# Performance work log

Hardware: AMD Instinct MI355X
Metric: run time of the kernel (lower is better)

The kernel has to match this reference:

```python
import jax, jax.numpy as jnp
import numpy as np

TANH_CLIP = 10.0
TEMP = 1.0


def setup_inputs() -> dict:
    key = jax.random.key(0)
    ks = jax.random.split(key, 8)
    B, N, E, H, SC = 1024, 1000, 128, 8, 256
    dk = E // H
    context = jax.random.normal(ks[0], (B, 1, E), dtype=jnp.float32)
    step_context = jax.random.normal(ks[1], (B, 1, SC), dtype=jnp.float32)
    # scale weights so tanh/softmax stay in a sane numeric range
    W_step = jax.random.normal(ks[2], (E, SC), dtype=jnp.float32) * 0.05
    glimpse_K = jax.random.normal(ks[3], (H, B, 1, N, dk), dtype=jnp.float32)
    glimpse_V = jax.random.normal(ks[4], (H, B, 1, N, dk), dtype=jnp.float32)
    logit_K = jax.random.normal(ks[5], (B, 1, N, E), dtype=jnp.float32)
    W_out = jax.random.normal(ks[6], (E, E), dtype=jnp.float32) * 0.05
    mask = jax.random.randint(ks[7], (B, 1, N), 0, 2).astype(bool)
    mask = mask.at[:, :, 0].set(False)  # guarantee at least one feasible node
    return {"context": context, "step_context": step_context, "W_step": W_step,
            "glimpse_K": glimpse_K, "glimpse_V": glimpse_V, "logit_K": logit_K,
            "W_out": W_out, "mask": mask}


def reference(context, step_context, W_step, glimpse_K, glimpse_V, logit_K, W_out, mask):
    B, S, E = context.shape          # S = num_steps = 1
    H = glimpse_K.shape[0]
    dk = E // H
    neg_inf = jnp.float32(-jnp.inf)
    # query = context_node_projected + project_step_context(step_context)
    query = context + jnp.einsum('bsc,ec->bse', step_context, W_step)  # [B,S,E]
    # split heads: glimpse_Q -> [H,B,S,dk] (the singleton q-dim of the torch code is folded)
    Q = query.reshape(B, S, H, dk).transpose(2, 0, 1, 3)
    # compatibility [H,B,S,N]
    compat = jnp.einsum('hbsk,hbsnk->hbsn', Q, glimpse_K) / jnp.sqrt(jnp.float32(dk))
    compat = jnp.where(mask[None], neg_inf, compat)       # mask_inner
    attn = jax.nn.softmax(compat, axis=-1)
    heads = jnp.einsum('hbsn,hbsnk->hbsk', attn, glimpse_V)  # [H,B,S,dk]
    glimpse = heads.transpose(1, 2, 0, 3).reshape(B, S, E)   # concat heads
    glimpse = jnp.einsum('bse,oe->bso', glimpse, W_out)      # project_out
    # logits against logit_K  [B,S,N]
    logits = jnp.einsum('bse,bsne->bsn', glimpse, logit_K) / jnp.sqrt(jnp.float32(E))
    logits = jnp.tanh(logits) * jnp.float32(TANH_CLIP)       # tanh clipping
    logits = jnp.where(mask, neg_inf, logits)                # mask_logits
    log_p = jax.nn.log_softmax(logits / jnp.float32(TEMP), axis=-1)
    return log_p
```

## Files before the change

### kernel.cpp

```cpp
#include <hip/hip_runtime.h>
#include <hip/hip_bf16.h>
#include <math.h>

#define NB  1024
#define NN  1000
#define NE  128
#define NH  8
#define NDK 16
#define NSC 256

__global__ __launch_bounds__(128)
void query_kernel(const float* __restrict__ ctx, const float* __restrict__ stepc,
                  const float* __restrict__ Wstep, float* __restrict__ q_ws)
{
    const int b = blockIdx.x, t = threadIdx.x;
    __shared__ float sc[NSC];
    sc[t] = stepc[b * NSC + t];
    sc[t + 128] = stepc[b * NSC + t + 128];
    __syncthreads();
    float acc = ctx[b * NE + t];
    const float4* w4 = reinterpret_cast<const float4*>(Wstep + t * NSC);
    #pragma unroll 8
    for (int c4 = 0; c4 < NSC / 4; ++c4) {
        float4 w = w4[c4];
        acc += sc[4*c4] * w.x + sc[4*c4+1] * w.y + sc[4*c4+2] * w.z + sc[4*c4+3] * w.w;
    }
    q_ws[b * NE + t] = acc;
}

__global__ __launch_bounds__(256)
void attn_kernel(const float* __restrict__ q_ws, const float* __restrict__ gK,
                 const float* __restrict__ gV, const unsigned char* __restrict__ mask,
                 float* __restrict__ heads_ws)
{
    const int bid = blockIdx.x;
    const int h = bid >> 10;
    const int b = bid & (NB - 1);
    const int t = threadIdx.x;
    const int w = t >> 6, lane = t & 63;

    __shared__ float wmax[4], wsum[4], wred[64];
    __shared__ int mtype;

    if (t == 0) {
        const unsigned int* mi = reinterpret_cast<const unsigned int*>(mask);
        int ok = 1;
        for (int i = 0; i < 64; ++i) ok = ok && (mi[i] <= 1u);
        mtype = ok;
    }
    __syncthreads();
    const int m_i32 = mtype;
    const int* mask_i = reinterpret_cast<const int*>(mask);

    const float4* q4 = reinterpret_cast<const float4*>(q_ws + b * NE + h * NDK);
    float4 q0 = q4[0], q1 = q4[1], q2 = q4[2], q3 = q4[3];

    const float* Kbase = gK + ((size_t)h * NB + b) * NN * NDK;
    const float* Vbase = gV + ((size_t)h * NB + b) * NN * NDK;

    float sc[4];
    #pragma unroll
    for (int i = 0; i < 4; ++i) {
        const int n = t + i * 256;
        float v = -INFINITY;
        if (n < NN) {
            bool mk = m_i32 ? (mask_i[b * NN + n] != 0) : (mask[b * NN + n] != 0);
            if (!mk) {
                const float4* k4 = reinterpret_cast<const float4*>(Kbase + (size_t)n * NDK);
                float4 k0 = k4[0], k1 = k4[1], k2 = k4[2], k3 = k4[3];
                float acc = k0.x*q0.x + k0.y*q0.y + k0.z*q0.z + k0.w*q0.w
                          + k1.x*q1.x + k1.y*q1.y + k1.z*q1.z + k1.w*q1.w
                          + k2.x*q2.x + k2.y*q2.y + k2.z*q2.z + k2.w*q2.w
                          + k3.x*q3.x + k3.y*q3.y + k3.z*q3.z + k3.w*q3.w;
                v = acc * 0.25f;
            }
        }
        sc[i] = v;
    }

    float m = fmaxf(fmaxf(sc[0], sc[1]), fmaxf(sc[2], sc[3]));
    #pragma unroll
    for (int off = 32; off > 0; off >>= 1) m = fmaxf(m, __shfl_down(m, off));
    if (lane == 0) wmax[w] = m;
    __syncthreads();
    const float M = fmaxf(fmaxf(wmax[0], wmax[1]), fmaxf(wmax[2], wmax[3]));

    float e[4], s = 0.f;
    #pragma unroll
    for (int i = 0; i < 4; ++i) { e[i] = expf(sc[i] - M); s += e[i]; }
    #pragma unroll
    for (int off = 32; off > 0; off >>= 1) s += __shfl_down(s, off);
    if (lane == 0) wsum[w] = s;
    __syncthreads();
    const float rinv = 1.0f / (wsum[0] + wsum[1] + wsum[2] + wsum[3]);

    float acc[16];
    #pragma unroll
    for (int k = 0; k < 16; ++k) acc[k] = 0.f;
    #pragma unroll
    for (int i = 0; i < 4; ++i) {
        const int n = t + i * 256;
        const float p = e[i];
        if (n < NN && p != 0.f) {
            const float4* v4 = reinterpret_cast<const float4*>(Vbase + (size_t)n * NDK);
            float4 v0 = v4[0], v1 = v4[1], v2 = v4[2], v3 = v4[3];
            acc[0]+=p*v0.x; acc[1]+=p*v0.y; acc[2]+=p*v0.z; acc[3]+=p*v0.w;
            acc[4]+=p*v1.x; acc[5]+=p*v1.y; acc[6]+=p*v1.z; acc[7]+=p*v1.w;
            acc[8]+=p*v2.x; acc[9]+=p*v2.y; acc[10]+=p*v2.z; acc[11]+=p*v2.w;
            acc[12]+=p*v3.x; acc[13]+=p*v3.y; acc[14]+=p*v3.z; acc[15]+=p*v3.w;
        }
    }
    #pragma unroll
    for (int k = 0; k < 16; ++k) {
        float a = acc[k];
        #pragma unroll
        for (int off = 32; off > 0; off >>= 1) a += __shfl_down(a, off);
        acc[k] = a;
    }
    if (lane < 16) wred[w * 16 + lane] = acc[lane];
    __syncthreads();
    if (lane == 0) {
        #pragma unroll
        for (int k = 0; k < 16; ++k) wred[w * 16 + k] = acc[k];
    }
    __syncthreads();
    if (t < NDK) {
        float r = wred[t] + wred[16 + t] + wred[32 + t] + wred[48 + t];
        heads_ws[b * NE + h * NDK + t] = r * rinv;
    }
}

__global__ __launch_bounds__(256)
void logits_kernel(const float* __restrict__ heads_ws, const float* __restrict__ Wout,
                   const float* __restrict__ lK, const unsigned char* __restrict__ mask,
                   __hip_bfloat16* __restrict__ out)
{
    const int b = blockIdx.x, t = threadIdx.x;
    __shared__ __align__(16) float g[NE];
    __shared__ __align__(16) float gout[NE];
    __shared__ __align__(16) float llds[NN];
    __shared__ __align__(16) float red[256];
    __shared__ float Mv, Sv;
    __shared__ int mtype;

    if (t == 0) {
        const unsigned int* mi = reinterpret_cast<const unsigned int*>(mask);
        int ok = 1;
        for (int i = 0; i < 64; ++i) ok = ok && (mi[i] <= 1u);
        mtype = ok;
    }
    if (t < NE) g[t] = heads_ws[b * NE + t];
    __syncthreads();
    const int m_i32 = mtype;
    const int* mask_i = reinterpret_cast<const int*>(mask);

    if (t < NE) {
        float acc = 0.f;
        const float4* w4 = reinterpret_cast<const float4*>(Wout + t * NE);
        const float4* g4 = reinterpret_cast<const float4*>(g);
        #pragma unroll 8
        for (int e4 = 0; e4 < NE / 4; ++e4) {
            float4 wv = w4[e4]; float4 gg = g4[e4];
            acc += wv.x*gg.x + wv.y*gg.y + wv.z*gg.z + wv.w*gg.w;
        }
        gout[t] = acc;
    }
    __syncthreads();

    for (int n = t; n < NN; n += 256) {
        bool mk = m_i32 ? (mask_i[b * NN + n] != 0) : (mask[b * NN + n] != 0);
        float val;
        if (mk) {
            val = -3.0e38f;
        } else {
            const float4* lk4 = reinterpret_cast<const float4*>(lK + ((size_t)b * NN + n) * NE);
            const float4* go4 = reinterpret_cast<const float4*>(gout);
            float acc = 0.f;
            #pragma unroll 8
            for (int e4 = 0; e4 < NE / 4; ++e4) {
                float4 lv = lk4[e4]; float4 gv = go4[e4];
                acc += lv.x*gv.x + lv.y*gv.y + lv.z*gv.z + lv.w*gv.w;
            }
            val = tanhf(acc * 0.08838834764831845f) * 10.0f;
        }
        llds[n] = val;
    }
    __syncthreads();

    float m = -INFINITY;
    for (int n = t; n < NN; n += 256) m = fmaxf(m, llds[n]);
    red[t] = m;
    __syncthreads();
    for (int s2 = 128; s2 > 0; s2 >>= 1) {
        if (t < s2) red[t] = fmaxf(red[t], red[t + s2]);
        __syncthreads();
    }
    if (t == 0) Mv = red[0];
    __syncthreads();
    const float M = Mv;
    float s = 0.f;
    for (int n = t; n < NN; n += 256) s += expf(llds[n] - M);
    red[t] = s;
    __syncthreads();
    for (int s2 = 128; s2 > 0; s2 >>= 1) {
        if (t < s2) red[t] += red[t + s2];
        __syncthreads();
    }
    if (t == 0) Sv = logf(red[0]);
    __syncthreads();
    const float LS = M + Sv;
    for (int n = t; n < NN; n += 256) {
        out[(size_t)b * NN + n] = __float2bfloat16(llds[n] - LS);
    }
}

__global__ __launch_bounds__(256, 4)
void evrp_decoder_fused(const float* __restrict__ ctx, const float* __restrict__ stepc,
                        const float* __restrict__ Wstep, const float* __restrict__ gK,
                        const float* __restrict__ gV, const float* __restrict__ lK,
                        const float* __restrict__ Wout, const unsigned char* __restrict__ mask,
                        __hip_bfloat16* __restrict__ out)
{
    const int b = blockIdx.x;
    const int t = threadIdx.x;
    __shared__ __align__(16) float q[NE];
    __shared__ __align__(16) float sc_l[NH * NN];
    __shared__ __align__(16) float g[NE];
    __shared__ __align__(16) float gout[NE];
    __shared__ __align__(16) float red[256];
    __shared__ __align__(16) float ovl[1024];
    __shared__ float mh[NH];
    __shared__ float rinv[NH];
    __shared__ float Mv, Sv;
    __shared__ int mtype;

    if (t == 0) {
        const unsigned int* mi = reinterpret_cast<const unsigned int*>(mask);
        int ok = 1;
        for (int i = 0; i < 64; ++i) ok = ok && (mi[i] <= 1u);
        mtype = ok;
    }
    red[t] = stepc[b * NSC + t];
    __syncthreads();
    const int m_i32 = mtype;
    if (t < NE) {
        float acc = ctx[b * NE + t];
        const float4* w4 = reinterpret_cast<const float4*>(Wstep + t * NSC);
        #pragma unroll 8
        for (int c4 = 0; c4 < NSC / 4; ++c4) {
            float4 w = w4[c4];
            acc += red[c4*4+0]*w.x + red[c4*4+1]*w.y + red[c4*4+2]*w.z + red[c4*4+3]*w.w;
        }
        q[t] = acc;
    }
    __syncthreads();
    const int* mask_i = reinterpret_cast<const int*>(mask);
    for (int n = t; n < NN; n += 256) {
        bool mk = m_i32 ? (mask_i[b * NN + n] != 0) : (mask[b * NN + n] != 0);
        if (mk) {
            #pragma unroll
            for (int h = 0; h < NH; ++h) sc_l[h * NN + n] = -INFINITY;
        } else {
            #pragma unroll
            for (int h = 0; h < NH; ++h) {
                const float4* k4 = reinterpret_cast<const float4*>(gK + (((size_t)h*NB + b)*NN + n)*NDK);
                const float4* q4 = reinterpret_cast<const float4*>(q + h * NDK);
                float acc = 0.f;
                #pragma unroll
                for (int i = 0; i < 4; ++i) {
                    float4 kv = k4[i]; float4 qv = q4[i];
                    acc += kv.x*qv.x + kv.y*qv.y + kv.z*qv.z + kv.w*qv.w;
                }
                sc_l[h * NN + n] = acc * 0.25f;
            }
        }
    }
    __syncthreads();
    {
        const int h = t >> 5, i = t & 31;
        float m = -INFINITY;
        for (int n = i; n < NN; n += 32) m = fmaxf(m, sc_l[h * NN + n]);
        red[t] = m;
        __syncthreads();
        if (t < NH) {
            float mm = -INFINITY;
            for (int i2 = 0; i2 < 32; ++i2) mm = fmaxf(mm, red[t * 32 + i2]);
            mh[t] = mm;
        }
        __syncthreads();
        const float mhh = mh[h];
        float s = 0.f;
        for (int n = i; n < NN; n += 32) {
            float ev = expf(sc_l[h * NN + n] - mhh);
            sc_l[h * NN + n] = ev;
            s += ev;
        }
        red[t] = s;
        __syncthreads();
        if (t < NH) {
            float ss = 0.f;
            for (int i2 = 0; i2 < 32; ++i2) ss += red[t * 32 + i2];
            rinv[t] = 1.0f / ss;
        }
        __syncthreads();
    }
    {
        float4* hp4 = reinterpret_cast<float4*>(ovl);
        const int h = t >> 5, rem = t & 31, kq = rem >> 3, j = rem & 7;
        const float* vbase = gV + (((size_t)h * NB + b) * NN) * NDK + kq * 4;
        float4 acc = {0.f, 0.f, 0.f, 0.f};
        for (int n = j; n < NN; n += 8) {
            float p = sc_l[h * NN + n];
            if (p != 0.f) {
                float4 v = *reinterpret_cast<const float4*>(vbase + (size_t)n * NDK);
                acc.x += p*v.x; acc.y += p*v.y; acc.z += p*v.z; acc.w += p*v.w;
            }
        }
        hp4[(h * 4 + kq) * 8 + j] = acc;
    }
    __syncthreads();
    if (t < NE) {
        const int h = t >> 4, k = t & 15, kq = k >> 2, kc = k & 3;
        float s = 0.f;
        #pragma unroll
        for (int j = 0; j < 8; ++j) s += ovl[((h * 4 + kq) * 8 + j) * 4 + kc];
        g[t] = s * rinv[h];
    }
    __syncthreads();
    if (t < NE) {
        float acc = 0.f;
        const float4* w4 = reinterpret_cast<const float4*>(Wout + t * NE);
        const float4* g4 = reinterpret_cast<const float4*>(g);
        #pragma unroll 8
        for (int e4 = 0; e4 < NE / 4; ++e4) {
            float4 w = w4[e4]; float4 gg = g4[e4];
            acc += w.x*gg.x + w.y*gg.y + w.z*gg.z + w.w*gg.w;
        }
        gout[t] = acc;
    }
    __syncthreads();
    float* llds = ovl;
    for (int n = t; n < NN; n += 256) {
        bool mk = m_i32 ? (mask_i[b * NN + n] != 0) : (mask[b * NN + n] != 0);
        float val;
        if (mk) val = -INFINITY;
        else {
            const float4* lk4 = reinterpret_cast<const float4*>(lK + ((size_t)b * NN + n) * NE);
            const float4* go4 = reinterpret_cast<const float4*>(gout);
            float acc = 0.f;
            #pragma unroll 8
            for (int e4 = 0; e4 < NE / 4; ++e4) {
                float4 lv = lk4[e4]; float4 gv = go4[e4];
                acc += lv.x*gv.x + lv.y*gv.y + lv.z*gv.z + lv.w*gv.w;
            }
            val = tanhf(acc * 0.08838834764831845f) * 10.0f;
        }
        llds[n] = val;
    }
    __syncthreads();
    {
        float m = -INFINITY;
        for (int n = t; n < NN; n += 256) m = fmaxf(m, llds[n]);
        red[t] = m;
        __syncthreads();
        for (int s2 = 128; s2 > 0; s2 >>= 1) {
            if (t < s2) red[t] = fmaxf(red[t], red[t + s2]);
            __syncthreads();
        }
        if (t == 0) Mv = red[0];
        __syncthreads();
        const float M = Mv;
        float s = 0.f;
        for (int n = t; n < NN; n += 256) s += expf(llds[n] - M);
        red[t] = s;
        __syncthreads();
        for (int s2 = 128; s2 > 0; s2 >>= 1) {
            if (t < s2) red[t] += red[t + s2];
            __syncthreads();
        }
        if (t == 0) Sv = logf(red[0]);
        __syncthreads();
        const float LS = M + Sv;
        for (int n = t; n < NN; n += 256) {
            float l = llds[n];
            float r = (l == -INFINITY) ? -3.0e38f : (l - LS);
            out[(size_t)b * NN + n] = __float2bfloat16(r);
        }
    }
}

extern "C" void kernel_launch(void* const* d_in, const int* in_sizes, int n_in,
                              void* d_out, int out_size, void* d_ws, size_t ws_size,
                              hipStream_t stream) {
    const float* ctx   = (const float*)d_in[0];
    const float* stepc = (const float*)d_in[1];
    const float* Wstep = (const float*)d_in[2];
    const float* gK    = (const float*)d_in[3];
    const float* gV    = (const float*)d_in[4];
    const float* lK    = (const float*)d_in[5];
    const float* Wout  = (const float*)d_in[6];
    const unsigned char* mask = (const unsigned char*)d_in[7];
    __hip_bfloat16* out = (__hip_bfloat16*)d_out;

    const size_t need = (size_t)NB * NE * 4 * 2;
    if (ws_size >= need) {
        float* q_ws     = (float*)d_ws;
        float* heads_ws = q_ws + (size_t)NB * NE;
        query_kernel <<<dim3(NB),      dim3(128), 0, stream>>>(ctx, stepc, Wstep, q_ws);
        attn_kernel  <<<dim3(NB * NH), dim3(256), 0, stream>>>(q_ws, gK, gV, mask, heads_ws);
        logits_kernel<<<dim3(NB),      dim3(256), 0, stream>>>(heads_ws, Wout, lK, mask, out);
    } else {
        evrp_decoder_fused<<<dim3(NB), dim3(256), 0, stream>>>(
            ctx, stepc, Wstep, gK, gV, lK, Wout, mask, out);
    }
}
```

Before: 222.7 us.

## Fuse query projection into attention, use nontemporal loads, register-resident logits softmax

Drops the separate query kernel: each attention block now computes its own 16-element head slice of the query from step_context and W_step, saving a launch and a workspace round trip at the cost of some redundant projection work. The attention kernel switches to contiguous per-thread node chunks with vectorised mask loads and nontemporal loads for K and V. The logits kernel moves to 512 threads, keeps logits in registers instead of LDS, uses wave shuffle reductions in place of LDS tree reductions, and streams logit_K with nontemporal loads. The contiguous per-thread chunking makes adjacent lanes read addresses 256 bytes apart, which may hurt coalescing.

```diff
diff --git a/kernel.cpp b/kernel.cpp
--- a/kernel.cpp
+++ b/kernel.cpp
@@ -9,28 +9,17 @@
 #define NDK 16
 #define NSC 256
 
-__global__ __launch_bounds__(128)
-void query_kernel(const float* __restrict__ ctx, const float* __restrict__ stepc,
-                  const float* __restrict__ Wstep, float* __restrict__ q_ws)
-{
-    const int b = blockIdx.x, t = threadIdx.x;
-    __shared__ float sc[NSC];
-    sc[t] = stepc[b * NSC + t];
-    sc[t + 128] = stepc[b * NSC + t + 128];
-    __syncthreads();
-    float acc = ctx[b * NE + t];
-    const float4* w4 = reinterpret_cast<const float4*>(Wstep + t * NSC);
-    #pragma unroll 8
-    for (int c4 = 0; c4 < NSC / 4; ++c4) {
-        float4 w = w4[c4];
-        acc += sc[4*c4] * w.x + sc[4*c4+1] * w.y + sc[4*c4+2] * w.z + sc[4*c4+3] * w.w;
-    }
-    q_ws[b * NE + t] = acc;
+typedef __attribute__((ext_vector_type(4))) float f32x4;
+
+__device__ __forceinline__ f32x4 ntload4(const float* p) {
+    return __builtin_nontemporal_load(reinterpret_cast<const f32x4*>(p));
 }
 
 __global__ __launch_bounds__(256)
-void attn_kernel(const float* __restrict__ q_ws, const float* __restrict__ gK,
-                 const float* __restrict__ gV, const unsigned char* __restrict__ mask,
+void attn_kernel(const float* __restrict__ ctx, const float* __restrict__ stepc,
+                 const float* __restrict__ Wstep,
+                 const float* __restrict__ gK, const float* __restrict__ gV,
+                 const unsigned char* __restrict__ mask,
                  float* __restrict__ heads_ws)
 {
     const int bid = blockIdx.x;
@@ -39,9 +28,12 @@
     const int t = threadIdx.x;
     const int w = t >> 6, lane = t & 63;
 
+    __shared__ __align__(16) float scx[NSC];
+    __shared__ __align__(16) float qh[NDK];
     __shared__ float wmax[4], wsum[4], wred[64];
     __shared__ int mtype;
 
+    scx[t] = stepc[b * NSC + t];
     if (t == 0) {
         const unsigned int* mi = reinterpret_cast<const unsigned int*>(mask);
         int ok = 1;
@@ -50,30 +42,51 @@
     }
     __syncthreads();
     const int m_i32 = mtype;
-    const int* mask_i = reinterpret_cast<const int*>(mask);
-
-    const float4* q4 = reinterpret_cast<const float4*>(q_ws + b * NE + h * NDK);
-    float4 q0 = q4[0], q1 = q4[1], q2 = q4[2], q3 = q4[3];
-
-    const float* Kbase = gK + ((size_t)h * NB + b) * NN * NDK;
-    const float* Vbase = gV + ((size_t)h * NB + b) * NN * NDK;
-
+
+    if (t < NDK) {
+        const int row = h * NDK + t;
+        float acc = ctx[b * NE + row];
+        const float4* w4 = reinterpret_cast<const float4*>(Wstep + row * NSC);
+        const float4* s4 = reinterpret_cast<const float4*>(scx);
+        #pragma unroll 8
+        for (int c4 = 0; c4 < NSC / 4; ++c4) {
+            float4 wv = w4[c4]; float4 sv = s4[c4];
+            acc += wv.x*sv.x + wv.y*sv.y + wv.z*sv.z + wv.w*sv.w;
+        }
+        qh[t] = acc;
+    }
+    __syncthreads();
+
+    const f32x4* q4 = reinterpret_cast<const f32x4*>(qh);
+    const f32x4 qA = q4[0], qB = q4[1], qC = q4[2], qD = q4[3];
+
+    const int n0 = t * 4;
+    const bool live = (n0 < NN);
+    int mk[4] = {1, 1, 1, 1};
+    if (live) {
+        if (m_i32) {
+            int4 mv = *reinterpret_cast<const int4*>(
+                reinterpret_cast<const int*>(mask) + (size_t)b * NN + n0);
+            mk[0] = mv.x; mk[1] = mv.y; mk[2] = mv.z; mk[3] = mv.w;
+        } else {
+            uchar4 mv = *reinterpret_cast<const uchar4*>(mask + (size_t)b * NN + n0);
+            mk[0] = mv.x; mk[1] = mv.y; mk[2] = mv.z; mk[3] = mv.w;
+        }
+    }
+
+    const float* Kbase = gK + (((size_t)h * NB + b) * NN + n0) * NDK;
     float sc[4];
     #pragma unroll
     for (int i = 0; i < 4; ++i) {
-        const int n = t + i * 256;
         float v = -INFINITY;
-        if (n < NN) {
-            bool mk = m_i32 ? (mask_i[b * NN + n] != 0) : (mask[b * NN + n] != 0);
-            if (!mk) {
-                const float4* k4 = reinterpret_cast<const float4*>(Kbase + (size_t)n * NDK);
-                float4 k0 = k4[0], k1 = k4[1], k2 = k4[2], k3 = k4[3];
-                float acc = k0.x*q0.x + k0.y*q0.y + k0.z*q0.z + k0.w*q0.w
-                          + k1.x*q1.x + k1.y*q1.y + k1.z*q1.z + k1.w*q1.w
-                          + k2.x*q2.x + k2.y*q2.y + k2.z*q2.z + k2.w*q2.w
-                          + k3.x*q3.x + k3.y*q3.y + k3.z*q3.z + k3.w*q3.w;
-                v = acc * 0.25f;
-            }
+        if (live && !mk[i]) {
+            const float* kp = Kbase + i * NDK;
+            f32x4 k0 = ntload4(kp), k1 = ntload4(kp + 4), k2 = ntload4(kp + 8), k3 = ntload4(kp + 12);
+            float acc = k0.x*qA.x + k0.y*qA.y + k0.z*qA.z + k0.w*qA.w
+                      + k1.x*qB.x + k1.y*qB.y + k1.z*qB.z + k1.w*qB.w
+                      + k2.x*qC.x + k2.y*qC.y + k2.z*qC.z + k2.w*qC.w
+                      + k3.x*qD.x + k3.y*qD.y + k3.z*qD.z + k3.w*qD.w;
+            v = acc * 0.25f;
         }
         sc[i] = v;
     }
@@ -97,13 +110,13 @@
     float acc[16];
     #pragma unroll
     for (int k = 0; k < 16; ++k) acc[k] = 0.f;
+    const float* Vbase = gV + (((size_t)h * NB + b) * NN + n0) * NDK;
     #pragma unroll
     for (int i = 0; i < 4; ++i) {
-        const int n = t + i * 256;
         const float p = e[i];
-        if (n < NN && p != 0.f) {
-            const float4* v4 = reinterpret_cast<const float4*>(Vbase + (size_t)n * NDK);
-            float4 v0 = v4[0], v1 = v4[1], v2 = v4[2], v3 = v4[3];
+        if (p != 0.f) {
+            const float* vp = Vbase + i * NDK;
+            f32x4 v0 = ntload4(vp), v1 = ntload4(vp + 4), v2 = ntload4(vp + 8), v3 = ntload4(vp + 12);
             acc[0]+=p*v0.x; acc[1]+=p*v0.y; acc[2]+=p*v0.z; acc[3]+=p*v0.w;
             acc[4]+=p*v1.x; acc[5]+=p*v1.y; acc[6]+=p*v1.z; acc[7]+=p*v1.w;
             acc[8]+=p*v2.x; acc[9]+=p*v2.y; acc[10]+=p*v2.z; acc[11]+=p*v2.w;
@@ -117,8 +130,6 @@
         for (int off = 32; off > 0; off >>= 1) a += __shfl_down(a, off);
         acc[k] = a;
     }
-    if (lane < 16) wred[w * 16 + lane] = acc[lane];
-    __syncthreads();
     if (lane == 0) {
         #pragma unroll
         for (int k = 0; k < 16; ++k) wred[w * 16 + k] = acc[k];
@@ -130,17 +141,17 @@
     }
 }
 
-__global__ __launch_bounds__(256)
+__global__ __launch_bounds__(512, 8)
 void logits_kernel(const float* __restrict__ heads_ws, const float* __restrict__ Wout,
                    const float* __restrict__ lK, const unsigned char* __restrict__ mask,
                    __hip_bfloat16* __restrict__ out)
 {
     const int b = blockIdx.x, t = threadIdx.x;
+    const int w = t >> 6, lane = t & 63;
     __shared__ __align__(16) float g[NE];
     __shared__ __align__(16) float gout[NE];
-    __shared__ __align__(16) float llds[NN];
-    __shared__ __align__(16) float red[256];
-    __shared__ float Mv, Sv;
+    __shared__ float red[8];
+    __shared__ float Mv, LSv;
     __shared__ int mtype;
 
     if (t == 0) {
@@ -167,50 +178,58 @@
     }
     __syncthreads();
 
-    for (int n = t; n < NN; n += 256) {
-        bool mk = m_i32 ? (mask_i[b * NN + n] != 0) : (mask[b * NN + n] != 0);
-        float val;
-        if (mk) {
-            val = -3.0e38f;
-        } else {
-            const float4* lk4 = reinterpret_cast<const float4*>(lK + ((size_t)b * NN + n) * NE);
-            const float4* go4 = reinterpret_cast<const float4*>(gout);
-            float acc = 0.f;
-            #pragma unroll 8
-            for (int e4 = 0; e4 < NE / 4; ++e4) {
-                float4 lv = lk4[e4]; float4 gv = go4[e4];
-                acc += lv.x*gv.x + lv.y*gv.y + lv.z*gv.z + lv.w*gv.w;
+    const f32x4* go4 = reinterpret_cast<const f32x4*>(gout);
+    float lv[2] = {-3.0e38f, -3.0e38f};
+    #pragma unroll
+    for (int i = 0; i < 2; ++i) {
+        const int n = t + 512 * i;
+        if (n < NN) {
+            bool mkd = m_i32 ? (mask_i[b * NN + n] != 0) : (mask[b * NN + n] != 0);
+            if (!mkd) {
+                const float* lp = lK + ((size_t)b * NN + n) * NE;
+                float acc = 0.f;
+                #pragma unroll
+                for (int c4 = 0; c4 < NE / 4; ++c4) {
+                    f32x4 x = ntload4(lp + 4 * c4);
+                    f32x4 gv = go4[c4];
+                    acc += x.x*gv.x + x.y*gv.y + x.z*gv.z + x.w*gv.w;
+                }
+                lv[i] = tanhf(acc * 0.08838834764831845f) * 10.0f;
             }
-            val = tanhf(acc * 0.08838834764831845f) * 10.0f;
-        }
-        llds[n] = val;
-    }
-    __syncthreads();
-
-    float m = -INFINITY;
-    for (int n = t; n < NN; n += 256) m = fmaxf(m, llds[n]);
-    red[t] = m;
-    __syncthreads();
-    for (int s2 = 128; s2 > 0; s2 >>= 1) {
-        if (t < s2) red[t] = fmaxf(red[t], red[t + s2]);
-        __syncthreads();
-    }
-    if (t == 0) Mv = red[0];
+        }
+    }
+
+    float m = fmaxf(lv[0], lv[1]);
+    #pragma unroll
+    for (int off = 32; off > 0; off >>= 1) m = fmaxf(m, __shfl_down(m, off));
+    if (lane == 0) red[w] = m;
+    __syncthreads();
+    if (t == 0) {
+        float mm = red[0];
+        #pragma unroll
+        for (int i = 1; i < 8; ++i) mm = fmaxf(mm, red[i]);
+        Mv = mm;
+    }
     __syncthreads();
     const float M = Mv;
-    float s = 0.f;
-    for (int n = t; n < NN; n += 256) s += expf(llds[n] - M);
-    red[t] = s;
-    __syncthreads();
-    for (int s2 = 128; s2 > 0; s2 >>= 1) {
-        if (t < s2) red[t] += red[t + s2];
-        __syncthreads();
-    }
-    if (t == 0) Sv = logf(red[0]);
-    __syncthreads();
-    const float LS = M + Sv;
-    for (int n = t; n < NN; n += 256) {
-        out[(size_t)b * NN + n] = __float2bfloat16(llds[n] - LS);
+    float s = expf(lv[0] - M) + expf(lv[1] - M);
+    #pragma unroll
+    for (int off = 32; off > 0; off >>= 1) s += __shfl_down(s, off);
+    if (lane == 0) red[w] = s;
+    __syncthreads();
+    if (t == 0) {
+        float ss = 0.f;
+        #pragma unroll
+        for (int i = 0; i < 8; ++i) ss += red[i];
+        LSv = M + logf(ss);
+    }
+    __syncthreads();
+    const float LS = LSv;
+    #pragma unroll
+    for (int i = 0; i < 2; ++i) {
+        const int n = t + 512 * i;
+        if (n < NN)
+            out[(size_t)b * NN + n] = __float2bfloat16(lv[i] - LS);
     }
 }
 
@@ -350,8 +369,8 @@
             float acc = 0.f;
             #pragma unroll 8
             for (int e4 = 0; e4 < NE / 4; ++e4) {
-                float4 lv = lk4[e4]; float4 gv = go4[e4];
-                acc += lv.x*gv.x + lv.y*gv.y + lv.z*gv.z + lv.w*gv.w;
+                float4 lvv = lk4[e4]; float4 gv = go4[e4];
+                acc += lvv.x*gv.x + lvv.y*gv.y + lvv.z*gv.z + lvv.w*gv.w;
             }
             val = tanhf(acc * 0.08838834764831845f) * 10.0f;
         }
@@ -402,13 +421,11 @@
     const unsigned char* mask = (const unsigned char*)d_in[7];
     __hip_bfloat16* out = (__hip_bfloat16*)d_out;
 
-    const size_t need = (size_t)NB * NE * 4 * 2;
+    const size_t need = (size_t)NB * NE * 4;
     if (ws_size >= need) {
-        float* q_ws     = (float*)d_ws;
-        float* heads_ws = q_ws + (size_t)NB * NE;
-        query_kernel <<<dim3(NB),      dim3(128), 0, stream>>>(ctx, stepc, Wstep, q_ws);
-        attn_kernel  <<<dim3(NB * NH), dim3(256), 0, stream>>>(q_ws, gK, gV, mask, heads_ws);
-        logits_kernel<<<dim3(NB),      dim3(256), 0, stream>>>(heads_ws, Wout, lK, mask, out);
+        float* heads_ws = (float*)d_ws;
+        attn_kernel  <<<dim3(NB * NH), dim3(256), 0, stream>>>(ctx, stepc, Wstep, gK, gV, mask, heads_ws);
+        logits_kernel<<<dim3(NB),      dim3(512), 0, stream>>>(heads_ws, Wout, lK, mask, out);
     } else {
         evrp_decoder_fused<<<dim3(NB), dim3(256), 0, stream>>>(
             ctx, stepc, Wstep, gK, gV, lK, Wout, mask, out);
```

Result: slower. 486.7 us (+118.6%).
